# Kernel optimization log

Measured on AMD Instinct MI355X. Metric: run time of the kernel, lower is better.

## Reference

```python
import jax, jax.numpy as jnp
import numpy as np

B, N, C = 8, 2000, 81
MAX_INST = 100
MIN_CONF = 0.7
NMS_THR = 0.3
BBOX_STD = jnp.array([0.1, 0.1, 0.2, 0.2], dtype=jnp.float32)
CLASS_OFFSET = 4.0  # per-class box offset so one NMS == per-class NMS


def setup_inputs() -> dict:
    key = jax.random.key(0)
    k1, k2, k3, k4 = jax.random.split(key, 4)
    # well-formed normalized rois: y1<y2, x1<x2
    ctr = jax.random.uniform(k1, (B, N, 2), minval=0.2, maxval=0.8)
    sz = jax.random.uniform(k2, (B, N, 2), minval=0.02, maxval=0.3)
    y1x1 = jnp.clip(ctr - 0.5 * sz, 0.0, 1.0)
    y2x2 = jnp.clip(ctr + 0.5 * sz, 0.0, 1.0)
    rois = jnp.concatenate([y1x1, y2x2], axis=-1).astype(jnp.float32)
    mrcnn_class = jax.nn.softmax(4.0 * jax.random.normal(k3, (B, N, C)), axis=-1).astype(jnp.float32)
    mrcnn_bbox = (0.1 * jax.random.normal(k4, (B, N, C, 4))).astype(jnp.float32)
    # meta: [image_id(1), orig_shape(3), image_shape(3), window(4), scale(1), active_class_ids(C)]
    meta_row = np.concatenate([
        np.array([0.0]), np.array([1024.0, 1024.0, 3.0]), np.array([1024.0, 1024.0, 3.0]),
        np.array([0.0, 0.0, 1024.0, 1024.0]), np.array([1.0]), np.ones(C)]).astype(np.float32)
    image_meta = jnp.broadcast_to(jnp.asarray(meta_row), (B, 12 + C))
    return {"rois": rois, "mrcnn_class": mrcnn_class, "mrcnn_bbox": mrcnn_bbox, "image_meta": image_meta}


def _apply_box_deltas(boxes, deltas):  # [N,4],[N,4]
    h = boxes[:, 2] - boxes[:, 0]
    w = boxes[:, 3] - boxes[:, 1]
    cy = boxes[:, 0] + 0.5 * h + deltas[:, 0] * h
    cx = boxes[:, 1] + 0.5 * w + deltas[:, 1] * w
    h = h * jnp.exp(deltas[:, 2])
    w = w * jnp.exp(deltas[:, 3])
    return jnp.stack([cy - 0.5 * h, cx - 0.5 * w, cy + 0.5 * h, cx + 0.5 * w], axis=1)


def _clip_boxes(boxes, window):  # window: [4]
    wy1, wx1, wy2, wx2 = window[0], window[1], window[2], window[3]
    y1 = jnp.clip(boxes[:, 0], wy1, wy2)
    x1 = jnp.clip(boxes[:, 1], wx1, wx2)
    y2 = jnp.clip(boxes[:, 2], wy1, wy2)
    x2 = jnp.clip(boxes[:, 3], wx1, wx2)
    return jnp.stack([y1, x1, y2, x2], axis=1)


def _pairwise_iou(b):  # [N,4] -> [N,N]
    area = (b[:, 2] - b[:, 0]) * (b[:, 3] - b[:, 1])
    iy = jnp.maximum(0.0, jnp.minimum(b[:, None, 2], b[None, :, 2]) - jnp.maximum(b[:, None, 0], b[None, :, 0]))
    ix = jnp.maximum(0.0, jnp.minimum(b[:, None, 3], b[None, :, 3]) - jnp.maximum(b[:, None, 1], b[None, :, 1]))
    inter = iy * ix
    return inter / (area[:, None] + area[None, :] - inter + 1e-12)


def _refine_one(rois, probs, deltas, window):
    n = rois.shape[0]
    class_ids = jnp.argmax(probs, axis=1)                      # [N]
    idx = jnp.arange(n)
    scores = probs[idx, class_ids]                              # [N]
    ds = deltas[idx, class_ids] * BBOX_STD                      # [N,4]
    refined = _clip_boxes(_apply_box_deltas(rois, ds), window)  # [N,4]
    valid = (class_ids > 0) & (scores >= MIN_CONF)
    # per-class NMS via class-offset trick (classes can never overlap)
    off_boxes = refined + CLASS_OFFSET * class_ids.astype(jnp.float32)[:, None]
    order = jnp.argsort(-jnp.where(valid, scores, -1.0))
    b_sorted = off_boxes[order]
    iou = _pairwise_iou(b_sorted)                               # [N,N]
    pos = jnp.arange(n)

    def body(keep, i):
        sup = keep[i] & (iou[i] > NMS_THR) & (pos > i)
        return keep & ~sup, None

    keep_sorted, _ = jax.lax.scan(body, valid[order], pos)
    keep = jnp.zeros(n, bool).at[order].set(keep_sorted)
    # per-class cap at MAX_INST (mirror max_output_size of per-class NMS)
    same = class_ids[:, None] == class_ids[None, :]
    before = (scores[None, :] > scores[:, None]) | ((scores[None, :] == scores[:, None]) & (pos[None, :] < pos[:, None]))
    rank = jnp.sum(keep[None, :] & same & before, axis=1)
    keep = keep & (rank < MAX_INST)
    # global top-k by score, pad with zeros
    masked = jnp.where(keep, scores, -1.0)
    top_scores, top_idx = jax.lax.top_k(masked, MAX_INST)
    valid_out = top_scores > 0.0
    det = jnp.concatenate([
        refined[top_idx],
        class_ids[top_idx].astype(jnp.float32)[:, None],
        scores[top_idx][:, None]], axis=1)                      # [MAX_INST,6]
    return jnp.where(valid_out[:, None], det, 0.0)


def reference(rois, mrcnn_class, mrcnn_bbox, image_meta):
    # normalize per-image window using image_shape of first image (as in original)
    image_shape = image_meta[0, 4:7]
    h, w = image_shape[0], image_shape[1]
    scale = jnp.stack([h, w, h, w]) - 1.0
    shift = jnp.array([0.0, 0.0, 1.0, 1.0], dtype=jnp.float32)
    window = (image_meta[:, 7:11] - shift) / scale              # [B,4]
    det = jax.vmap(_refine_one)(rois, mrcnn_class, mrcnn_bbox, window)
    return det.reshape(rois.shape[0], MAX_INST, 6)
```

## Files before the change

kernel.cpp:

```cpp
#include <hip/hip_runtime.h>
#include <stdint.h>

#define Bn 8
#define Nn 2000
#define Cc 81
#define META_STRIDE (12 + Cc)
#define MAXI 100
#define MINCONF 0.7f
#define NMSTHR 0.3f
#define NPAD 2048
#define PB_ROIS 128
#define PSTRIDE 83

__device__ __forceinline__ uint32_t ford(float f) {
    uint32_t u = __float_as_uint(f);
    return (u & 0x80000000u) ? ~u : (u | 0x80000000u);
}

__device__ __forceinline__ unsigned long long shflx64(unsigned long long v, int lx) {
    unsigned int lo = (unsigned int)v, hi = (unsigned int)(v >> 32);
    lo = (unsigned int)__shfl_xor((int)lo, lx, 64);
    hi = (unsigned int)__shfl_xor((int)hi, lx, 64);
    return ((unsigned long long)hi << 32) | lo;
}

__global__ void __launch_bounds__(256)
k_prep(const float* __restrict__ rois,
       const float* __restrict__ probs,
       const float* __restrict__ bbox,
       const float* __restrict__ meta,
       float* __restrict__ refined,
       float* __restrict__ score,
       int* __restrict__ cls,
       unsigned long long* __restrict__ keys) {
    __shared__ float sp[PB_ROIS * PSTRIDE];
    int tid  = threadIdx.x;
    int base = blockIdx.x * PB_ROIS;

    const float* gp = probs + (size_t)base * Cc;
    const int total = PB_ROIS * Cc;
    int r = tid / Cc, c = tid - r * Cc;
    for (int idx = tid; idx < total; idx += 256) {
        sp[r * PSTRIDE + c] = gp[idx];
        r += 3; c += 13;
        if (c >= Cc) { c -= Cc; r += 1; }
    }
    __syncthreads();

    int row  = tid >> 1;
    int half = tid & 1;
    const float* sr = sp + row * PSTRIDE;
    int   c0 = half ? 41 : 0;
    int   c1 = half ? Cc : 41;
    float v  = sr[c0];
    int   cb = c0;
    for (int cc2 = c0 + 1; cc2 < c1; ++cc2) {
        float x = sr[cc2];
        if (x > v) { v = x; cb = cc2; }
    }
    float vo = __shfl_xor(v, 1, 64);
    int   co = __shfl_xor(cb, 1, 64);
    float vA = half ? vo : v;   int cA = half ? co : cb;
    float vB = half ? v  : vo;  int cB = half ? cb : co;
    float sbest;  int cbest;
    if (vB > vA) { sbest = vB; cbest = cB; }
    else         { sbest = vA; cbest = cA; }

    if (half) return;
    int t = base + row;

    float4 d4 = reinterpret_cast<const float4*>(bbox)[(size_t)t * Cc + cbest];
    float dy = d4.x * 0.1f, dx = d4.y * 0.1f, dh = d4.z * 0.2f, dw = d4.w * 0.2f;

    float4 r4 = reinterpret_cast<const float4*>(rois)[t];
    float y1 = r4.x, x1 = r4.y, y2 = r4.z, x2 = r4.w;
    float h = y2 - y1, w = x2 - x1;
    float cy = y1 + 0.5f * h + dy * h;
    float cx = x1 + 0.5f * w + dx * w;
    h = h * expf(dh);
    w = w * expf(dw);
    float ny1 = cy - 0.5f * h, nx1 = cx - 0.5f * w;
    float ny2 = cy + 0.5f * h, nx2 = cx + 0.5f * w;

    int b = t / Nn;
    float sy = meta[4] - 1.0f, sx = meta[5] - 1.0f;
    const float* mb = meta + (size_t)b * META_STRIDE;
    float wy1 = mb[7] / sy;
    float wx1 = mb[8] / sx;
    float wy2 = (mb[9]  - 1.0f) / sy;
    float wx2 = (mb[10] - 1.0f) / sx;

    ny1 = fminf(fmaxf(ny1, wy1), wy2);
    nx1 = fminf(fmaxf(nx1, wx1), wx2);
    ny2 = fminf(fmaxf(ny2, wy1), wy2);
    nx2 = fminf(fmaxf(nx2, wx1), wx2);

    reinterpret_cast<float4*>(refined)[t] = float4{ny1, nx1, ny2, nx2};
    score[t] = sbest;
    cls[t]   = cbest;

    int i = t - b * Nn;
    bool valid = (cbest > 0) && (sbest >= MINCONF);
    float ks = valid ? sbest : -1.0f;
    keys[t] = ((unsigned long long)ford(ks) << 32) |
              (unsigned long long)(0xFFFFFFFFu - (uint32_t)i);
}

__global__ void __launch_bounds__(1024, 1)
k_batch(const unsigned long long* __restrict__ keys,
        const float* __restrict__ refined,
        const float* __restrict__ score,
        const int* __restrict__ cls,
        float* __restrict__ out) {
    __shared__ unsigned long long sk[NPAD];
    __shared__ float4 sboxL[Nn];
    __shared__ unsigned long long intraw[64];
    __shared__ unsigned long long extw[16];
    __shared__ int klist[128];
    __shared__ int sV, sNk;

    int b = blockIdx.x, tid = threadIdx.x;
    int wid = tid >> 6, lane = tid & 63;
    int e0 = tid << 1;

    const unsigned long long* kb = keys + (size_t)b * Nn;
    unsigned long long a = (e0     < Nn) ? kb[e0]     : 0ull;
    unsigned long long bv = (e0 + 1 < Nn) ? kb[e0 + 1] : 0ull;
    if (tid == 0) { sV = 0; sNk = 0; }

    for (int k = 2; k <= 128; k <<= 1) {
        bool desc = ((e0 & k) == 0);
        for (int j = k >> 1; j >= 2; j >>= 1) {
            int lx = j >> 1;
            bool keepmax = (desc == ((lane & lx) == 0));
            unsigned long long oa = shflx64(a, lx);
            unsigned long long ob = shflx64(bv, lx);
            a  = keepmax ? (a  > oa ? a  : oa) : (a  < oa ? a  : oa);
            bv = keepmax ? (bv > ob ? bv : ob) : (bv < ob ? bv : ob);
        }
        bool sw = desc ? (a < bv) : (a > bv);
        if (sw) { unsigned long long t2 = a; a = bv; bv = t2; }
    }
    sk[e0] = a; sk[e0 + 1] = bv;
    __syncthreads();

    for (int k = 256; k <= NPAD; k <<= 1) {
        for (int j = k >> 1; j >= 128; j >>= 1) {
            #pragma unroll
            for (int rep = 0; rep < 2; ++rep) {
                int t = tid + (rep << 10);
                int ixj = t ^ j;
                if (ixj > t) {
                    unsigned long long x = sk[t], y = sk[ixj];
                    bool desc = ((t & k) == 0);
                    if (desc ? (x < y) : (x > y)) { sk[t] = y; sk[ixj] = x; }
                }
            }
            __syncthreads();
        }
        a = sk[e0]; bv = sk[e0 + 1];
        bool desc = ((e0 & k) == 0);
        #pragma unroll
        for (int lx = 32; lx >= 1; lx >>= 1) {
            bool keepmax = (desc == ((lane & lx) == 0));
            unsigned long long oa = shflx64(a, lx);
            unsigned long long ob = shflx64(bv, lx);
            a  = keepmax ? (a  > oa ? a  : oa) : (a  < oa ? a  : oa);
            bv = keepmax ? (bv > ob ? bv : ob) : (bv < ob ? bv : ob);
        }
        bool sw = desc ? (a < bv) : (a > bv);
        if (sw) { unsigned long long t2 = a; a = bv; bv = t2; }
        sk[e0] = a; sk[e0 + 1] = bv;
        __syncthreads();
    }

    for (int t = tid; t < Nn; t += 1024) {
        bool v0 = (sk[t] >> 63) != 0ull;
        bool v1 = (t + 1 < Nn) ? ((sk[t + 1] >> 63) != 0ull) : false;
        if (v0 && !v1) sV = t + 1;
    }
    __syncthreads();
    int V = sV;

    for (int t = tid; t < V; t += 1024) {
        uint32_t oi = 0xFFFFFFFFu - (uint32_t)(sk[t] & 0xFFFFFFFFull);
        int gi = b * Nn + (int)oi;
        float off = 4.0f * (float)cls[gi];
        float4 rf = reinterpret_cast<const float4*>(refined)[gi];
        sboxL[t] = float4{rf.x + off, rf.y + off, rf.z + off, rf.w + off};
    }
    __syncthreads();

    int nblocks = (V + 63) >> 6;
    for (int t = 0; t < nblocks; ++t) {
        int base = t << 6;
        int nb = V - base; if (nb > 64) nb = 64;
        int K = sNk;

        float4 cb = (lane < nb) ? sboxL[base + lane] : float4{0.f, 0.f, 0.f, 0.f};
        float a2 = (cb.z - cb.x) * (cb.w - cb.y);

        bool supext = false;
        for (int k = wid; k < K; k += 16) {
            float4 kbx = sboxL[klist[k]];
            float ar = (kbx.z - kbx.x) * (kbx.w - kbx.y);
            float iy = fmaxf(0.0f, fminf(kbx.z, cb.z) - fmaxf(kbx.x, cb.x));
            float ix = fmaxf(0.0f, fminf(kbx.w, cb.w) - fmaxf(kbx.y, cb.y));
            float inter = iy * ix;
            float iou = inter / (ar + a2 - inter + 1e-12f);
            supext |= (lane < nb) && (iou > NMSTHR);
        }
        unsigned long long bw = __ballot(supext);
        if (lane == 0) extw[wid] = bw;

        #pragma unroll
        for (int s = 0; s < 4; ++s) {
            int rr = (wid << 2) + s;
            bool sup = false;
            if (rr < nb && lane < nb && lane > rr) {
                float4 rb = sboxL[base + rr];
                float ar = (rb.z - rb.x) * (rb.w - rb.y);
                float iy = fmaxf(0.0f, fminf(rb.z, cb.z) - fmaxf(rb.x, cb.x));
                float ix = fmaxf(0.0f, fminf(rb.w, cb.w) - fmaxf(rb.y, cb.y));
                float inter = iy * ix;
                float iou = inter / (ar + a2 - inter + 1e-12f);
                sup = iou > NMSTHR;
            }
            unsigned long long rb2 = __ballot(sup);
            if (lane == 0) intraw[rr] = rb2;
        }
        __syncthreads();

        if (wid == 0) {
            unsigned long long intra_l = intraw[lane];
            unsigned long long e = (lane < 16) ? extw[lane] : 0ull;
            #pragma unroll
            for (int m = 8; m >= 1; m >>= 1) e |= __shfl_xor(e, m, 64);
            e = __shfl(e, 0, 64);

            int nk = K;
            bool alive = (lane < nb) && !((e >> lane) & 1ull);
            unsigned long long candm = __ballot(alive);
            while (candm) {
                int i = __builtin_ctzll(candm);
                if (lane == 0) klist[nk] = base + i;
                ++nk;
                if (nk >= MAXI) break;
                unsigned long long rowi = __shfl(intra_l, i, 64);
                alive = alive && !((rowi >> lane) & 1ull);
                candm = __ballot(alive) & ~((2ull << i) - 1ull);
            }
            if (lane == 0) sNk = nk;
        }
        __syncthreads();
        if (sNk >= MAXI) break;
    }

    int ne = sNk < MAXI ? sNk : MAXI;
    for (int r = tid; r < ne; r += 1024) {
        int pos = klist[r];
        uint32_t oi = 0xFFFFFFFFu - (uint32_t)(sk[pos] & 0xFFFFFFFFull);
        int gi = b * Nn + (int)oi;
        float4 rf = reinterpret_cast<const float4*>(refined)[gi];
        float* orow = out + ((size_t)b * MAXI + r) * 6;
        orow[0] = rf.x;
        orow[1] = rf.y;
        orow[2] = rf.z;
        orow[3] = rf.w;
        orow[4] = (float)cls[gi];
        orow[5] = score[gi];
    }
    for (int tt = ne * 6 + tid; tt < MAXI * 6; tt += 1024)
        out[(size_t)b * MAXI * 6 + tt] = 0.0f;
}

extern "C" void kernel_launch(void* const* d_in, const int* in_sizes, int n_in,
                              void* d_out, int out_size, void* d_ws, size_t ws_size,
                              hipStream_t stream) {
    const float* rois  = (const float*)d_in[0];
    const float* probs = (const float*)d_in[1];
    const float* bbox  = (const float*)d_in[2];
    const float* meta  = (const float*)d_in[3];
    float* out = (float*)d_out;

    const int BN = Bn * Nn;
    char* ws = (char*)d_ws;
    size_t off = 0;
    auto alloc = [&](size_t bytes) {
        void* p = ws + off;
        off += (bytes + 255) & ~(size_t)255;
        return p;
    };
    float*              refined = (float*)              alloc((size_t)BN * 4 * sizeof(float));
    float*              score   = (float*)              alloc((size_t)BN * sizeof(float));
    int*                cls     = (int*)                alloc((size_t)BN * sizeof(int));
    unsigned long long* keys    = (unsigned long long*) alloc((size_t)BN * sizeof(unsigned long long));
    (void)ws_size; (void)in_sizes; (void)n_in; (void)out_size;

    k_prep<<<BN / PB_ROIS, 256, 0, stream>>>(rois, probs, bbox, meta,
                                             refined, score, cls, keys);
    k_batch<<<Bn, 1024, 0, stream>>>(keys, refined, score, cls, out);
}
```

Baseline: 45.91 us.

## Precompute intra-block IoU masks and pipeline external suppression with greedy NMS scan

```diff
diff --git a/kernel.cpp b/kernel.cpp
--- a/kernel.cpp
+++ b/kernel.cpp
@@ -114,19 +114,20 @@
         float* __restrict__ out) {
     __shared__ unsigned long long sk[NPAD];
     __shared__ float4 sboxL[Nn];
-    __shared__ unsigned long long intraw[64];
-    __shared__ unsigned long long extw[16];
+    __shared__ unsigned long long intraM[NPAD];
+    __shared__ unsigned long long extbuf[2][16];
     __shared__ int klist[128];
-    __shared__ int sV, sNk;
+    __shared__ int sKpub[2];
+    __shared__ int sV, sNk, sDone;
 
     int b = blockIdx.x, tid = threadIdx.x;
     int wid = tid >> 6, lane = tid & 63;
     int e0 = tid << 1;
 
     const unsigned long long* kb = keys + (size_t)b * Nn;
-    unsigned long long a = (e0     < Nn) ? kb[e0]     : 0ull;
+    unsigned long long a  = (e0     < Nn) ? kb[e0]     : 0ull;
     unsigned long long bv = (e0 + 1 < Nn) ? kb[e0 + 1] : 0ull;
-    if (tid == 0) { sV = 0; sNk = 0; }
+    if (tid == 0) { sV = 0; sNk = 0; sDone = 0; sKpub[0] = 0; sKpub[1] = 0; }
 
     for (int k = 2; k <= 128; k <<= 1) {
         bool desc = ((e0 & k) == 0);
@@ -192,69 +193,108 @@
     __syncthreads();
 
     int nblocks = (V + 63) >> 6;
-    for (int t = 0; t < nblocks; ++t) {
-        int base = t << 6;
+    for (int tb = wid; tb < nblocks; tb += 16) {
+        int base = tb << 6;
+        int pos = base + lane;
+        float4 cb = (pos < V) ? sboxL[pos] : float4{0.f, 0.f, 0.f, 0.f};
+        float a2 = (cb.z - cb.x) * (cb.w - cb.y);
         int nb = V - base; if (nb > 64) nb = 64;
-        int K = sNk;
-
-        float4 cb = (lane < nb) ? sboxL[base + lane] : float4{0.f, 0.f, 0.f, 0.f};
-        float a2 = (cb.z - cb.x) * (cb.w - cb.y);
-
-        bool supext = false;
-        for (int k = wid; k < K; k += 16) {
-            float4 kbx = sboxL[klist[k]];
-            float ar = (kbx.z - kbx.x) * (kbx.w - kbx.y);
-            float iy = fmaxf(0.0f, fminf(kbx.z, cb.z) - fmaxf(kbx.x, cb.x));
-            float ix = fmaxf(0.0f, fminf(kbx.w, cb.w) - fmaxf(kbx.y, cb.y));
-            float inter = iy * ix;
-            float iou = inter / (ar + a2 - inter + 1e-12f);
-            supext |= (lane < nb) && (iou > NMSTHR);
-        }
-        unsigned long long bw = __ballot(supext);
-        if (lane == 0) extw[wid] = bw;
-
-        #pragma unroll
-        for (int s = 0; s < 4; ++s) {
-            int rr = (wid << 2) + s;
+        for (int r = 0; r < nb; ++r) {
+            float rx = __shfl(cb.x, r, 64);
+            float ry = __shfl(cb.y, r, 64);
+            float rz = __shfl(cb.z, r, 64);
+            float rw = __shfl(cb.w, r, 64);
+            float ar = (rz - rx) * (rw - ry);
             bool sup = false;
-            if (rr < nb && lane < nb && lane > rr) {
-                float4 rb = sboxL[base + rr];
-                float ar = (rb.z - rb.x) * (rb.w - rb.y);
-                float iy = fmaxf(0.0f, fminf(rb.z, cb.z) - fmaxf(rb.x, cb.x));
-                float ix = fmaxf(0.0f, fminf(rb.w, cb.w) - fmaxf(rb.y, cb.y));
+            if (lane > r && pos < V) {
+                float iy = fmaxf(0.0f, fminf(rz, cb.z) - fmaxf(rx, cb.x));
+                float ix = fmaxf(0.0f, fminf(rw, cb.w) - fmaxf(ry, cb.y));
                 float inter = iy * ix;
                 float iou = inter / (ar + a2 - inter + 1e-12f);
                 sup = iou > NMSTHR;
             }
-            unsigned long long rb2 = __ballot(sup);
-            if (lane == 0) intraw[rr] = rb2;
+            unsigned long long ball = __ballot(sup);
+            if (lane == 0) intraM[base + r] = ball;
+        }
+    }
+    __syncthreads();
+
+    int prevP = 0, lastP = 0;
+    for (int t = 0; t <= nblocks; ++t) {
+        if (sDone) break;
+        if (wid != 0) {
+            if (t < nblocks) {
+                int base = t << 6;
+                int nb = V - base; if (nb > 64) nb = 64;
+                float4 cb = (lane < nb) ? sboxL[base + lane]
+                                        : float4{0.f, 0.f, 0.f, 0.f};
+                float a2 = (cb.z - cb.x) * (cb.w - cb.y);
+                int Kold = sKpub[t & 1];
+                bool supext = false;
+                for (int k = wid - 1; k < Kold; k += 15) {
+                    float4 kbx = sboxL[klist[k]];
+                    float ar = (kbx.z - kbx.x) * (kbx.w - kbx.y);
+                    float iy = fmaxf(0.0f, fminf(kbx.z, cb.z) - fmaxf(kbx.x, cb.x));
+                    float ix = fmaxf(0.0f, fminf(kbx.w, cb.w) - fmaxf(kbx.y, cb.y));
+                    float inter = iy * ix;
+                    float iou = inter / (ar + a2 - inter + 1e-12f);
+                    supext |= (lane < nb) && (iou > NMSTHR);
+                }
+                unsigned long long bw = __ballot(supext);
+                if (lane == 0) extbuf[t & 1][wid] = bw;
+            }
+        } else {
+            int bt = t - 1;
+            if (bt >= 0 && bt < nblocks) {
+                int base = bt << 6;
+                int nb = V - base; if (nb > 64) nb = 64;
+
+                unsigned long long e =
+                    (lane >= 1 && lane < 16) ? extbuf[bt & 1][lane] : 0ull;
+                #pragma unroll
+                for (int m = 32; m >= 1; m >>= 1) e |= shflx64(e, m);
+
+                int dn = lastP - prevP;
+                float4 cbr = (lane < nb) ? sboxL[base + lane]
+                                         : float4{0.f, 0.f, 0.f, 0.f};
+                float a2r = (cbr.z - cbr.x) * (cbr.w - cbr.y);
+                float4 kb4 = float4{0.f, 0.f, 0.f, 0.f};
+                if (lane < dn) kb4 = sboxL[klist[prevP + lane]];
+                for (int d = 0; d < dn; ++d) {
+                    float kx = __shfl(kb4.x, d, 64);
+                    float ky = __shfl(kb4.y, d, 64);
+                    float kz = __shfl(kb4.z, d, 64);
+                    float kw = __shfl(kb4.w, d, 64);
+                    float ar = (kz - kx) * (kw - ky);
+                    float iy = fmaxf(0.0f, fminf(kz, cbr.z) - fmaxf(kx, cbr.x));
+                    float ix = fmaxf(0.0f, fminf(kw, cbr.w) - fmaxf(ky, cbr.y));
+                    float inter = iy * ix;
+                    float iou = inter / (ar + a2r - inter + 1e-12f);
+                    e |= __ballot((lane < nb) && (iou > NMSTHR));
+                }
+
+                unsigned long long myintra = intraM[base + lane];
+                bool alive = (lane < nb) && !((e >> lane) & 1ull);
+                unsigned long long candm = __ballot(alive);
+                int nk = lastP;
+                while (candm) {
+                    int i = __builtin_ctzll(candm);
+                    if (lane == 0) klist[nk] = base + i;
+                    ++nk;
+                    if (nk >= MAXI) { if (lane == 0) sDone = 1; break; }
+                    unsigned long long rowi = __shfl(myintra, i, 64);
+                    alive = alive && !((rowi >> lane) & 1ull);
+                    candm = __ballot(alive) & ~((2ull << i) - 1ull);
+                }
+                prevP = lastP; lastP = nk;
+                if (lane == 0) sKpub[(t + 1) & 1] = nk;
+            }
+            if (t == nblocks && lane == 0) sNk = lastP;
         }
         __syncthreads();
-
-        if (wid == 0) {
-            unsigned long long intra_l = intraw[lane];
-            unsigned long long e = (lane < 16) ? extw[lane] : 0ull;
-            #pragma unroll
-            for (int m = 8; m >= 1; m >>= 1) e |= __shfl_xor(e, m, 64);
-            e = __shfl(e, 0, 64);
-
-            int nk = K;
-            bool alive = (lane < nb) && !((e >> lane) & 1ull);
-            unsigned long long candm = __ballot(alive);
-            while (candm) {
-                int i = __builtin_ctzll(candm);
-                if (lane == 0) klist[nk] = base + i;
-                ++nk;
-                if (nk >= MAXI) break;
-                unsigned long long rowi = __shfl(intra_l, i, 64);
-                alive = alive && !((rowi >> lane) & 1ull);
-                candm = __ballot(alive) & ~((2ull << i) - 1ull);
-            }
-            if (lane == 0) sNk = nk;
-        }
-        __syncthreads();
-        if (sNk >= MAXI) break;
-    }
+    }
+    if (sDone && wid == 0 && lane == 0) sNk = lastP;
+    __syncthreads();
 
     int ne = sNk < MAXI ? sNk : MAXI;
     for (int r = tid; r < ne; r += 1024) {
```

After: 70.51 us. 1.54x slower.

## Run greedy NMS in a single wavefront with per-class kept lists

Applied to the files above, without the earlier changes.

```diff
diff --git a/kernel.cpp b/kernel.cpp
--- a/kernel.cpp
+++ b/kernel.cpp
@@ -11,6 +11,7 @@
 #define NPAD 2048
 #define PB_ROIS 128
 #define PSTRIDE 83
+#define KCAP 104
 
 __device__ __forceinline__ uint32_t ford(float f) {
     uint32_t u = __float_as_uint(f);
@@ -114,8 +115,9 @@
         float* __restrict__ out) {
     __shared__ unsigned long long sk[NPAD];
     __shared__ float4 sboxL[Nn];
-    __shared__ unsigned long long intraw[64];
-    __shared__ unsigned long long extw[16];
+    __shared__ unsigned short scls[Nn];
+    __shared__ unsigned short kidx[Cc * KCAP];
+    __shared__ int kcnt[Cc];
     __shared__ int klist[128];
     __shared__ int sV, sNk;
 
@@ -124,9 +126,10 @@
     int e0 = tid << 1;
 
     const unsigned long long* kb = keys + (size_t)b * Nn;
-    unsigned long long a = (e0     < Nn) ? kb[e0]     : 0ull;
+    unsigned long long a  = (e0     < Nn) ? kb[e0]     : 0ull;
     unsigned long long bv = (e0 + 1 < Nn) ? kb[e0 + 1] : 0ull;
     if (tid == 0) { sV = 0; sNk = 0; }
+    if (tid < Cc) kcnt[tid] = 0;
 
     for (int k = 2; k <= 128; k <<= 1) {
         bool desc = ((e0 & k) == 0);
@@ -185,76 +188,69 @@
     for (int t = tid; t < V; t += 1024) {
         uint32_t oi = 0xFFFFFFFFu - (uint32_t)(sk[t] & 0xFFFFFFFFull);
         int gi = b * Nn + (int)oi;
-        float off = 4.0f * (float)cls[gi];
+        int c  = cls[gi];
+        float off = 4.0f * (float)c;
         float4 rf = reinterpret_cast<const float4*>(refined)[gi];
         sboxL[t] = float4{rf.x + off, rf.y + off, rf.z + off, rf.w + off};
-    }
-    __syncthreads();
-
-    int nblocks = (V + 63) >> 6;
-    for (int t = 0; t < nblocks; ++t) {
-        int base = t << 6;
-        int nb = V - base; if (nb > 64) nb = 64;
-        int K = sNk;
-
-        float4 cb = (lane < nb) ? sboxL[base + lane] : float4{0.f, 0.f, 0.f, 0.f};
-        float a2 = (cb.z - cb.x) * (cb.w - cb.y);
-
-        bool supext = false;
-        for (int k = wid; k < K; k += 16) {
-            float4 kbx = sboxL[klist[k]];
-            float ar = (kbx.z - kbx.x) * (kbx.w - kbx.y);
-            float iy = fmaxf(0.0f, fminf(kbx.z, cb.z) - fmaxf(kbx.x, cb.x));
-            float ix = fmaxf(0.0f, fminf(kbx.w, cb.w) - fmaxf(kbx.y, cb.y));
-            float inter = iy * ix;
-            float iou = inter / (ar + a2 - inter + 1e-12f);
-            supext |= (lane < nb) && (iou > NMSTHR);
-        }
-        unsigned long long bw = __ballot(supext);
-        if (lane == 0) extw[wid] = bw;
-
-        #pragma unroll
-        for (int s = 0; s < 4; ++s) {
-            int rr = (wid << 2) + s;
+        scls[t]  = (unsigned short)c;
+    }
+    __syncthreads();
+
+    if (wid == 0) {
+        int nblocks = (V + 63) >> 6;
+        int nk = 0;
+        bool done = false;
+        for (int t = 0; t < nblocks && !done; ++t) {
+            int base = t << 6;
+            int nb = V - base; if (nb > 64) nb = 64;
+            int pos = base + lane;
+            float4 cb = (lane < nb) ? sboxL[pos] : float4{0.f, 0.f, 0.f, 0.f};
+            int   myc = (lane < nb) ? (int)scls[pos] : 0;
+            float a2  = (cb.z - cb.x) * (cb.w - cb.y);
+
             bool sup = false;
-            if (rr < nb && lane < nb && lane > rr) {
-                float4 rb = sboxL[base + rr];
-                float ar = (rb.z - rb.x) * (rb.w - rb.y);
-                float iy = fmaxf(0.0f, fminf(rb.z, cb.z) - fmaxf(rb.x, cb.x));
-                float ix = fmaxf(0.0f, fminf(rb.w, cb.w) - fmaxf(rb.y, cb.y));
+            int cnt = (lane < nb) ? kcnt[myc] : 0;
+            for (int s = 0; s < cnt; ++s) {
+                int ki = (int)kidx[myc * KCAP + s];
+                float4 kbx = sboxL[ki];
+                float ar = (kbx.z - kbx.x) * (kbx.w - kbx.y);
+                float iy = fmaxf(0.0f, fminf(kbx.z, cb.z) - fmaxf(kbx.x, cb.x));
+                float ix = fmaxf(0.0f, fminf(kbx.w, cb.w) - fmaxf(kbx.y, cb.y));
                 float inter = iy * ix;
                 float iou = inter / (ar + a2 - inter + 1e-12f);
-                sup = iou > NMSTHR;
+                sup |= iou > NMSTHR;
             }
-            unsigned long long rb2 = __ballot(sup);
-            if (lane == 0) intraw[rr] = rb2;
-        }
-        __syncthreads();
-
-        if (wid == 0) {
-            unsigned long long intra_l = intraw[lane];
-            unsigned long long e = (lane < 16) ? extw[lane] : 0ull;
-            #pragma unroll
-            for (int m = 8; m >= 1; m >>= 1) e |= __shfl_xor(e, m, 64);
-            e = __shfl(e, 0, 64);
-
-            int nk = K;
-            bool alive = (lane < nb) && !((e >> lane) & 1ull);
+
+            bool alive = (lane < nb) && !sup;
             unsigned long long candm = __ballot(alive);
             while (candm) {
                 int i = __builtin_ctzll(candm);
-                if (lane == 0) klist[nk] = base + i;
+                int ic = __shfl(myc, i, 64);
+                if (lane == 0) {
+                    klist[nk] = base + i;
+                    int cc2 = kcnt[ic];
+                    kidx[ic * KCAP + cc2] = (unsigned short)(base + i);
+                    kcnt[ic] = cc2 + 1;
+                }
                 ++nk;
-                if (nk >= MAXI) break;
-                unsigned long long rowi = __shfl(intra_l, i, 64);
-                alive = alive && !((rowi >> lane) & 1ull);
+                if (nk >= MAXI) { done = true; break; }
+
+                float kx = __shfl(cb.x, i, 64);
+                float ky = __shfl(cb.y, i, 64);
+                float kz = __shfl(cb.z, i, 64);
+                float kw = __shfl(cb.w, i, 64);
+                float ar = (kz - kx) * (kw - ky);
+                float iy = fmaxf(0.0f, fminf(kz, cb.z) - fmaxf(kx, cb.x));
+                float ix = fmaxf(0.0f, fminf(kw, cb.w) - fmaxf(ky, cb.y));
+                float inter = iy * ix;
+                float iou = inter / (ar + a2 - inter + 1e-12f);
+                alive = alive && !(iou > NMSTHR);
                 candm = __ballot(alive) & ~((2ull << i) - 1ull);
             }
-            if (lane == 0) sNk = nk;
-        }
-        __syncthreads();
-        if (sNk >= MAXI) break;
-    }
+        }
+        if (lane == 0) sNk = nk;
+    }
+    __syncthreads();
 
     int ne = sNk < MAXI ? sNk : MAXI;
     for (int r = tid; r < ne; r += 1024) {
```

Result: slower. 55.75 us (+21.4%).
